# Kernel optimization log

Measured on AMD Instinct MI355X. Metric: run time of the kernel, lower is better.

Reference implementation:

```python
import jax, jax.numpy as jnp
import numpy as np

NODES_PER_GRAPH = 128


def _leaky(x):
    return jnp.where(x >= 0, x, 0.01 * x)


def _graph_conv(x, W, src, dst, w_e, n_nodes):
    # DGL GraphConv, norm='both', bias=False, with edge_weight.
    # Structural (unweighted) degrees, clamped to 1, as in DGL.
    ones = jnp.ones(src.shape[0], dtype=x.dtype)
    deg_out = jnp.clip(jax.ops.segment_sum(ones, src, num_segments=n_nodes), 1.0)
    deg_in = jnp.clip(jax.ops.segment_sum(ones, dst, num_segments=n_nodes), 1.0)
    x = x * (deg_out ** -0.5)[:, None]
    if W.shape[0] > W.shape[1]:  # in_feats > out_feats: project first (DGL order)
        x = x @ W
    msg = x[src] * w_e[:, None]                     # [E, d]
    agg = jax.ops.segment_sum(msg, dst, num_segments=n_nodes)
    agg = agg * (deg_in ** -0.5)[:, None]
    if W.shape[0] <= W.shape[1]:
        agg = agg @ W
    return agg


def setup_inputs() -> dict:
    key = jax.random.key(0)
    ks = jax.random.split(key, 8)
    N, E = 131072, 1048576
    in_feats, hidden, readout = 64, 256, 128
    return {
        "node_feats": jax.random.normal(ks[0], (N, in_feats), dtype=jnp.float32),
        "edge_weight": jax.random.uniform(ks[1], (E,), dtype=jnp.float32),
        "W1": jax.random.normal(ks[2], (in_feats, hidden), dtype=jnp.float32) * 0.1,
        "W2": jax.random.normal(ks[3], (hidden, readout), dtype=jnp.float32) * 0.05,
        "W_lin": jax.random.normal(ks[4], (readout, 64), dtype=jnp.float32) * 0.1,
        "W_cls": jax.random.normal(ks[5], (64, 16), dtype=jnp.float32) * 0.1,
        "edge_src": jax.random.randint(ks[6], (E,), 0, N, dtype=jnp.int32),
        "edge_dst": jax.random.randint(ks[7], (E,), 0, N, dtype=jnp.int32),
    }


def reference(node_feats, edge_weight, W1, W2, W_lin, W_cls, edge_src, edge_dst):
    N = node_feats.shape[0]
    G = N // NODES_PER_GRAPH
    h = _leaky(_graph_conv(node_feats, W1, edge_src, edge_dst, edge_weight, N))
    h = _leaky(_graph_conv(h, W2, edge_src, edge_dst, edge_weight, N))
    # mean_nodes readout over batched graphs of equal size
    gid = jnp.arange(N, dtype=jnp.int32) // NODES_PER_GRAPH
    pooled = jax.ops.segment_sum(h, gid, num_segments=G) / NODES_PER_GRAPH
    # linear -> dropout(eval: identity) -> classifier (no activation in head)
    return (pooled @ W_lin) @ W_cls
```

## Files before the change

kernel.cpp:

```cpp
#include <hip/hip_runtime.h>


constexpr int NPG = 128;
constexpr int F0  = 64;
constexpr int F1  = 256;
constexpr int F2  = 128;
constexpr int BMM = 64;
constexpr int H2  = 136;
constexpr int CAP = 40;
constexpr int NXCD = 8;

using bf16x8 = __attribute__((ext_vector_type(8))) short;
using f32x4  = __attribute__((ext_vector_type(4))) float;
using u16x8  = __attribute__((ext_vector_type(8))) unsigned short;

__device__ __forceinline__ float leaky(float x) {
    return (x >= 0.f) ? x : 0.01f * x;
}

__device__ __forceinline__ unsigned short f2bf(float x) {
    unsigned u = __float_as_uint(x);
    return (unsigned short)((u + 0x7FFFu + ((u >> 16) & 1u)) >> 16);
}
__device__ __forceinline__ float bf2f(unsigned short h) {
    return __uint_as_float(((unsigned)h) << 16);
}
__device__ __forceinline__ void split2(float x, unsigned short& hi, unsigned short& lo) {
    hi = f2bf(x);
    lo = f2bf(x - bf2f(hi));
}

__device__ __forceinline__ f32x4 mfma16(bf16x8 a, bf16x8 b, f32x4 c) {
    return __builtin_amdgcn_mfma_f32_16x16x32_bf16(a, b, c, 0, 0, 0);
}

__device__ __forceinline__ unsigned get_xcc() {
    unsigned xcc;
    asm("s_getreg_b32 %0, hwreg(HW_REG_XCC_ID)" : "=s"(xcc));
    return xcc & (NXCD - 1);
}


__global__ void k_count_fill(const int* __restrict__ src, const int* __restrict__ dst,
                             const float* __restrict__ we,
                             int* __restrict__ cnt_priv,
                             int* __restrict__ cnt_dst,
                             int2* __restrict__ slots, unsigned E, int N) {
    const unsigned xcc = get_xcc();
    unsigned e = blockIdx.x * 256u + threadIdx.x;
    if (e < E) {
        const int s = src[e], d = dst[e];
        const int pos = atomicAdd(&cnt_dst[d], 1);
        if (pos < CAP) slots[(size_t)d * CAP + pos] = make_int2(s, __float_as_int(we[e]));
        __hip_atomic_fetch_add(&cnt_priv[(size_t)xcc * N + s], 1,
                               __ATOMIC_RELAXED, __HIP_MEMORY_SCOPE_WORKGROUP);
    }
}

__global__ void k_finalize_deg(const int* __restrict__ cnt_priv,
                               const int* __restrict__ cnt_dst,
                               float* __restrict__ dinv_out, float* __restrict__ dinv_in,
                               int N) {
    int i = blockIdx.x * blockDim.x + threadIdx.x;
    if (i < N) {
        int c = 0;
#pragma unroll
        for (int x = 0; x < NXCD; ++x) c += cnt_priv[(size_t)x * N + i];
        dinv_out[i] = rsqrtf((float)max(c, 1));
        dinv_in[i]  = rsqrtf((float)max(cnt_dst[i], 1));
    }
}

__global__ void __launch_bounds__(256) k_scale_w(
        int2* __restrict__ slots, const int* __restrict__ cnt_dst,
        const float* __restrict__ dinv_out, int N) {
    int gid = blockIdx.x * 256 + threadIdx.x;
    int n = gid >> 3;
    int j0 = gid & 7;
    if (n >= N) return;
    const int cnt = min(cnt_dst[n], CAP);
    for (int j = j0; j < cnt; j += 8) {
        const size_t idx = (size_t)n * CAP + j;
        int2 p = slots[idx];
        p.y = __float_as_int(__int_as_float(p.y) * dinv_out[p.x]);
        slots[idx] = p;
    }
}

__global__ void k_wsplit1(const float* __restrict__ W1,
                          unsigned short* __restrict__ w1h, unsigned short* __restrict__ w1l) {
    int i = blockIdx.x * 256 + threadIdx.x;
    if (i < F1 * F0) {
        int n = i >> 6, k = i & 63;
        unsigned short h, l;
        split2(W1[k * F1 + n], h, l);
        w1h[i] = h; w1l[i] = l;
    }
}
__global__ void k_wsplit2(const float* __restrict__ W2,
                          unsigned short* __restrict__ w2h, unsigned short* __restrict__ w2l) {
    int i = blockIdx.x * 256 + threadIdx.x;
    if (i < F2 * F1) {
        int n = i >> 8, k = i & 255;
        unsigned short h, l;
        split2(W2[k * F2 + n], h, l);
        w2h[i] = h; w2l[i] = l;
    }
}

__global__ void __launch_bounds__(256) k_gather1(
        const float4* __restrict__ featsv, const int* __restrict__ cnt_dst,
        const int2* __restrict__ slots, const float* __restrict__ dinv_in,
        unsigned short* __restrict__ a1h, unsigned short* __restrict__ a1l, int N) {
    const int gid = blockIdx.x * 256 + threadIdx.x;
    const int n = gid >> 4;
    const int s = gid & 15;
    if (n >= N) return;
    const size_t b = (size_t)n * CAP;
    const int cnt = min(cnt_dst[n], CAP);
    float4 acc = make_float4(0.f, 0.f, 0.f, 0.f);
    int j = 0;
    for (; j + 4 <= cnt; j += 4) {
        const int2 p0 = slots[b + j], p1 = slots[b + j + 1];
        const int2 p2 = slots[b + j + 2], p3 = slots[b + j + 3];
        const float4 v0 = featsv[(size_t)p0.x * 16 + s];
        const float4 v1 = featsv[(size_t)p1.x * 16 + s];
        const float4 v2 = featsv[(size_t)p2.x * 16 + s];
        const float4 v3 = featsv[(size_t)p3.x * 16 + s];
        const float w0 = __int_as_float(p0.y), w1 = __int_as_float(p1.y);
        const float w2 = __int_as_float(p2.y), w3 = __int_as_float(p3.y);
        acc.x = fmaf(v0.x, w0, acc.x); acc.y = fmaf(v0.y, w0, acc.y);
        acc.z = fmaf(v0.z, w0, acc.z); acc.w = fmaf(v0.w, w0, acc.w);
        acc.x = fmaf(v1.x, w1, acc.x); acc.y = fmaf(v1.y, w1, acc.y);
        acc.z = fmaf(v1.z, w1, acc.z); acc.w = fmaf(v1.w, w1, acc.w);
        acc.x = fmaf(v2.x, w2, acc.x); acc.y = fmaf(v2.y, w2, acc.y);
        acc.z = fmaf(v2.z, w2, acc.z); acc.w = fmaf(v2.w, w2, acc.w);
        acc.x = fmaf(v3.x, w3, acc.x); acc.y = fmaf(v3.y, w3, acc.y);
        acc.z = fmaf(v3.z, w3, acc.z); acc.w = fmaf(v3.w, w3, acc.w);
    }
    for (; j < cnt; ++j) {
        const int2 p = slots[b + j];
        const float4 v = featsv[(size_t)p.x * 16 + s];
        const float w = __int_as_float(p.y);
        acc.x = fmaf(v.x, w, acc.x); acc.y = fmaf(v.y, w, acc.y);
        acc.z = fmaf(v.z, w, acc.z); acc.w = fmaf(v.w, w, acc.w);
    }
    const float din = dinv_in[n];
    ushort4 h4, l4;
    split2(acc.x * din, h4.x, l4.x);
    split2(acc.y * din, h4.y, l4.y);
    split2(acc.z * din, h4.z, l4.z);
    split2(acc.w * din, h4.w, l4.w);
    const size_t off = (size_t)n * 64 + s * 4;
    *(ushort4*)(a1h + off) = h4;
    *(ushort4*)(a1l + off) = l4;
}

__global__ void __launch_bounds__(256, 4) k_mfma_fused(
        const unsigned short* __restrict__ a1h, const unsigned short* __restrict__ a1l,
        const unsigned short* __restrict__ w1h, const unsigned short* __restrict__ w1l,
        const unsigned short* __restrict__ w2h, const unsigned short* __restrict__ w2l,
        unsigned short* __restrict__ x2b) {
    __shared__ unsigned short hhi[BMM][H2];
    __shared__ unsigned short hlo[BMM][H2];
    const int tid  = threadIdx.x;
    const int w    = tid >> 6;
    const int lane = tid & 63;
    const int r    = lane & 15;
    const int kg   = lane >> 4;
    const int base = blockIdx.x * BMM;

    f32x4 acc1[4][4] = {};
#pragma unroll
    for (int ks = 0; ks < 2; ++ks) {
        const int kk = ks * 32 + kg * 8;
        bf16x8 wh[4], wl[4];
#pragma unroll
        for (int j = 0; j < 4; ++j) {
            const int col = (j >> 1) * 128 + w * 32 + (j & 1) * 16 + r;
            wh[j] = *(const bf16x8*)(w1h + col * F0 + kk);
            wl[j] = *(const bf16x8*)(w1l + col * F0 + kk);
        }
#pragma unroll
        for (int mt = 0; mt < 4; ++mt) {
            const size_t aoff = (size_t)(base + mt * 16 + r) * F0 + kk;
            const bf16x8 ah = *(const bf16x8*)(a1h + aoff);
            const bf16x8 al = *(const bf16x8*)(a1l + aoff);
#pragma unroll
            for (int j = 0; j < 4; ++j) {
                acc1[mt][j] = mfma16(ah, wh[j], acc1[mt][j]);
                acc1[mt][j] = mfma16(ah, wl[j], acc1[mt][j]);
                acc1[mt][j] = mfma16(al, wh[j], acc1[mt][j]);
            }
        }
    }

    f32x4 acc2[4][2] = {};
    const int c2base = w * 32;
#pragma unroll
    for (int h = 0; h < 2; ++h) {
#pragma unroll
        for (int jn = 0; jn < 2; ++jn) {
            const int j = h * 2 + jn;
            const int lc = w * 32 + jn * 16 + r;
#pragma unroll
            for (int mt = 0; mt < 4; ++mt)
#pragma unroll
                for (int i = 0; i < 4; ++i) {
                    const int rl = mt * 16 + kg * 4 + i;
                    unsigned short hi_, lo_;
                    split2(leaky(acc1[mt][j][i]), hi_, lo_);
                    hhi[rl][lc] = hi_;
                    hlo[rl][lc] = lo_;
                }
        }
        __syncthreads();
#pragma unroll
        for (int ks = 0; ks < 4; ++ks) {
            const int lkk = ks * 32 + kg * 8;
            const int kglob = h * 128 + lkk;
            bf16x8 w2hv[2], w2lv[2];
#pragma unroll
            for (int nt = 0; nt < 2; ++nt) {
                const int col = c2base + nt * 16 + r;
                w2hv[nt] = *(const bf16x8*)(w2h + col * F1 + kglob);
                w2lv[nt] = *(const bf16x8*)(w2l + col * F1 + kglob);
            }
#pragma unroll
            for (int mt = 0; mt < 4; ++mt) {
                const int rl = mt * 16 + r;
                const bf16x8 ah = *(const bf16x8*)&hhi[rl][lkk];
                const bf16x8 al = *(const bf16x8*)&hlo[rl][lkk];
#pragma unroll
                for (int nt = 0; nt < 2; ++nt) {
                    acc2[mt][nt] = mfma16(ah, w2hv[nt], acc2[mt][nt]);
                    acc2[mt][nt] = mfma16(ah, w2lv[nt], acc2[mt][nt]);
                    acc2[mt][nt] = mfma16(al, w2hv[nt], acc2[mt][nt]);
                }
            }
        }
        __syncthreads();
    }

#pragma unroll
    for (int mt = 0; mt < 4; ++mt)
#pragma unroll
        for (int nt = 0; nt < 2; ++nt)
#pragma unroll
            for (int i = 0; i < 4; ++i) {
                const int row = base + mt * 16 + kg * 4 + i;
                const int col = c2base + nt * 16 + r;
                x2b[(size_t)row * F2 + col] = f2bf(acc2[mt][nt][i]);
            }
}

__global__ void __launch_bounds__(256) k_gather2_pool4(
        const ushort* __restrict__ x2b, const int* __restrict__ cnt_dst,
        const int2* __restrict__ slots, const float* __restrict__ dinv_in,
        float* __restrict__ pooled) {
    const int g = blockIdx.x >> 2;
    const int c = blockIdx.x & 3;
    const int t = threadIdx.x;
    const int q = t >> 2;
    const int s = t & 3;
    const int d8 = c * 4 + s;
    const u16x8* x2v = (const u16x8*)x2b;

    float pool[8];
#pragma unroll
    for (int k = 0; k < 8; ++k) pool[k] = 0.f;
    const int nbase = g * NPG;

#pragma unroll
    for (int i = 0; i < NPG; i += 64) {
        const int n = nbase + i + q;
        const size_t b = (size_t)n * CAP;
        const int cnt = min(cnt_dst[n], CAP);
        float a[8];
#pragma unroll
        for (int k = 0; k < 8; ++k) a[k] = 0.f;
        int j = 0;
        for (; j + 4 <= cnt; j += 4) {
            const int2 p0 = slots[b + j], p1 = slots[b + j + 1];
            const int2 p2 = slots[b + j + 2], p3 = slots[b + j + 3];
            const u16x8 u0 = x2v[(size_t)p0.x * 16 + d8];
            const u16x8 u1 = x2v[(size_t)p1.x * 16 + d8];
            const u16x8 u2 = x2v[(size_t)p2.x * 16 + d8];
            const u16x8 u3 = x2v[(size_t)p3.x * 16 + d8];
            const float w0 = __int_as_float(p0.y), w1 = __int_as_float(p1.y);
            const float w2 = __int_as_float(p2.y), w3 = __int_as_float(p3.y);
#pragma unroll
            for (int k = 0; k < 8; ++k) {
                a[k] = fmaf(bf2f(u0[k]), w0, a[k]);
                a[k] = fmaf(bf2f(u1[k]), w1, a[k]);
                a[k] = fmaf(bf2f(u2[k]), w2, a[k]);
                a[k] = fmaf(bf2f(u3[k]), w3, a[k]);
            }
        }
        for (; j < cnt; ++j) {
            const int2 p = slots[b + j];
            const float w = __int_as_float(p.y);
            const u16x8 u = x2v[(size_t)p.x * 16 + d8];
#pragma unroll
            for (int k = 0; k < 8; ++k) a[k] = fmaf(bf2f(u[k]), w, a[k]);
        }
        const float din = dinv_in[n];
#pragma unroll
        for (int k = 0; k < 8; ++k) pool[k] += leaky(a[k] * din);
    }

    __shared__ float pl[64][4][9];
#pragma unroll
    for (int k = 0; k < 8; ++k) pl[q][s][k] = pool[k];
    __syncthreads();
#pragma unroll
    for (int off = 32; off >= 1; off >>= 1) {
        if (q < off) {
#pragma unroll
            for (int k = 0; k < 8; ++k) {
                pool[k] += pl[q + off][s][k];
                pl[q][s][k] = pool[k];
            }
        }
        __syncthreads();
    }
    if (q == 0) {
        const float inv = 1.0f / NPG;
        float* dstp = pooled + (size_t)g * F2 + c * 32 + s * 8;
#pragma unroll
        for (int k = 0; k < 8; ++k) dstp[k] = pool[k] * inv;
    }
}

__global__ void __launch_bounds__(64) k_head(
        const float* __restrict__ pooled,
        const float* __restrict__ Wlin,
        const float* __restrict__ Wcls,
        float* __restrict__ out) {
    const int g = blockIdx.x;
    const int t = threadIdx.x;
    __shared__ float p[F2];
    __shared__ float tj[64];
    p[t]      = pooled[(size_t)g * F2 + t];
    p[t + 64] = pooled[(size_t)g * F2 + 64 + t];
    __syncthreads();
    float s = 0.f;
#pragma unroll
    for (int k = 0; k < F2; ++k) s = fmaf(p[k], Wlin[k * 64 + t], s);
    tj[t] = s;
    __syncthreads();
    if (t < 16) {
        float sum = 0.f;
#pragma unroll
        for (int j = 0; j < 64; ++j) sum = fmaf(tj[j], Wcls[j * 16 + t], sum);
        out[g * 16 + t] = sum;
    }
}

extern "C" void kernel_launch(void* const* d_in, const int* in_sizes, int n_in,
                              void* d_out, int out_size, void* d_ws, size_t ws_size,
                              hipStream_t stream) {
    const float* feats = (const float*)d_in[0];
    const float* we    = (const float*)d_in[1];
    const float* W1    = (const float*)d_in[2];
    const float* W2    = (const float*)d_in[3];
    const float* Wlin  = (const float*)d_in[4];
    const float* Wcls  = (const float*)d_in[5];
    const int*   src   = (const int*)d_in[6];
    const int*   dst   = (const int*)d_in[7];

    const int N = in_sizes[0] / F0;
    const unsigned E = (unsigned)in_sizes[1];
    const int G = N / NPG;

    float* out = (float*)d_out;

    int* ws_i = (int*)d_ws;
    size_t o = 0;
    auto align4 = [&]() { o = (o + 3) & ~(size_t)3; };
    int* cnt_dst = ws_i + o; o += N;
    int* cnt_priv = ws_i + o; o += (size_t)NXCD * N;
    float* dinv_out = (float*)(ws_i + o); o += N;
    float* dinv_in  = (float*)(ws_i + o); o += N;
    align4();
    int2* slots = (int2*)(ws_i + o); o += 2 * (size_t)N * CAP;
    unsigned short* a1h = (unsigned short*)(ws_i + o); o += (size_t)N * 32;
    unsigned short* a1l = (unsigned short*)(ws_i + o); o += (size_t)N * 32;
    unsigned short* x2b = (unsigned short*)(ws_i + o); o += (size_t)N * 64;
    unsigned short* w1h = (unsigned short*)(ws_i + o); o += (F1 * F0) / 2;
    unsigned short* w1l = (unsigned short*)(ws_i + o); o += (F1 * F0) / 2;
    unsigned short* w2h = (unsigned short*)(ws_i + o); o += (F2 * F1) / 2;
    unsigned short* w2l = (unsigned short*)(ws_i + o); o += (F2 * F1) / 2;
    align4();
    float* pooled = (float*)(ws_i + o); o += (size_t)G * F2;

    hipMemsetAsync(cnt_dst, 0, (size_t)(1 + NXCD) * N * sizeof(int), stream);

    k_count_fill<<<(E + 255) / 256, 256, 0, stream>>>(
        src, dst, we, cnt_priv, cnt_dst, slots, E, N);

    k_finalize_deg<<<(N + 255) / 256, 256, 0, stream>>>(
        cnt_priv, cnt_dst, dinv_out, dinv_in, N);

    k_scale_w<<<(N * 8 + 255) / 256, 256, 0, stream>>>(slots, cnt_dst, dinv_out, N);

    k_wsplit1<<<(F1 * F0 + 255) / 256, 256, 0, stream>>>(W1, w1h, w1l);
    k_wsplit2<<<(F2 * F1 + 255) / 256, 256, 0, stream>>>(W2, w2h, w2l);

    k_gather1<<<(N * 16 + 255) / 256, 256, 0, stream>>>(
        (const float4*)feats, cnt_dst, slots, dinv_in, a1h, a1l, N);

    k_mfma_fused<<<N / BMM, 256, 0, stream>>>(a1h, a1l, w1h, w1l, w2h, w2l, x2b);

    k_gather2_pool4<<<G * 4, 256, 0, stream>>>(
        x2b, cnt_dst, slots, dinv_in, pooled);
    k_head<<<G, 64, 0, stream>>>(pooled, Wlin, Wcls, out);
}
```

Before: 317.5 us.

## Gather layer-1 features from a bf16 copy and use nontemporal slot stores

Adds a pre-pass that converts the fp32 node features to bf16, and rewrites the first-layer gather to read 8 bf16 values per lane, which halves the bytes fetched per random neighbour row. The edge-slot fill now packs the source index and weight into one 64-bit value written with a nontemporal store. The change costs an extra conversion pass over the features and gives up precision on the layer-1 inputs, which were previously exact fp32 before the hi/lo split.

```diff
diff --git a/kernel.cpp b/kernel.cpp
--- a/kernel.cpp
+++ b/kernel.cpp
@@ -45,13 +45,17 @@
                              const float* __restrict__ we,
                              int* __restrict__ cnt_priv,
                              int* __restrict__ cnt_dst,
-                             int2* __restrict__ slots, unsigned E, int N) {
+                             long long* __restrict__ slots, unsigned E, int N) {
     const unsigned xcc = get_xcc();
     unsigned e = blockIdx.x * 256u + threadIdx.x;
     if (e < E) {
         const int s = src[e], d = dst[e];
         const int pos = atomicAdd(&cnt_dst[d], 1);
-        if (pos < CAP) slots[(size_t)d * CAP + pos] = make_int2(s, __float_as_int(we[e]));
+        if (pos < CAP) {
+            const long long v = ((long long)(unsigned)__float_as_int(we[e]) << 32)
+                              | (unsigned)s;
+            __builtin_nontemporal_store(v, &slots[(size_t)d * CAP + pos]);
+        }
         __hip_atomic_fetch_add(&cnt_priv[(size_t)xcc * N + s], 1,
                                __ATOMIC_RELAXED, __HIP_MEMORY_SCOPE_WORKGROUP);
     }
@@ -87,6 +91,19 @@
     }
 }
 
+__global__ void __launch_bounds__(256) k_feats_bf(
+        const float4* __restrict__ in, u16x8* __restrict__ out, int total8) {
+    int gid = blockIdx.x * 256 + threadIdx.x;
+    if (gid < total8) {
+        const float4 v0 = in[gid * 2];
+        const float4 v1 = in[gid * 2 + 1];
+        u16x8 r;
+        r[0] = f2bf(v0.x); r[1] = f2bf(v0.y); r[2] = f2bf(v0.z); r[3] = f2bf(v0.w);
+        r[4] = f2bf(v1.x); r[5] = f2bf(v1.y); r[6] = f2bf(v1.z); r[7] = f2bf(v1.w);
+        out[gid] = r;
+    }
+}
+
 __global__ void k_wsplit1(const float* __restrict__ W1,
                           unsigned short* __restrict__ w1h, unsigned short* __restrict__ w1l) {
     int i = blockIdx.x * 256 + threadIdx.x;
@@ -109,51 +126,55 @@
 }
 
 __global__ void __launch_bounds__(256) k_gather1(
-        const float4* __restrict__ featsv, const int* __restrict__ cnt_dst,
+        const u16x8* __restrict__ featsb,
+        const int* __restrict__ cnt_dst,
         const int2* __restrict__ slots, const float* __restrict__ dinv_in,
         unsigned short* __restrict__ a1h, unsigned short* __restrict__ a1l, int N) {
     const int gid = blockIdx.x * 256 + threadIdx.x;
-    const int n = gid >> 4;
-    const int s = gid & 15;
+    const int n = gid >> 3;
+    const int s = gid & 7;
     if (n >= N) return;
     const size_t b = (size_t)n * CAP;
     const int cnt = min(cnt_dst[n], CAP);
-    float4 acc = make_float4(0.f, 0.f, 0.f, 0.f);
+    float a[8];
+#pragma unroll
+    for (int k = 0; k < 8; ++k) a[k] = 0.f;
     int j = 0;
     for (; j + 4 <= cnt; j += 4) {
         const int2 p0 = slots[b + j], p1 = slots[b + j + 1];
         const int2 p2 = slots[b + j + 2], p3 = slots[b + j + 3];
-        const float4 v0 = featsv[(size_t)p0.x * 16 + s];
-        const float4 v1 = featsv[(size_t)p1.x * 16 + s];
-        const float4 v2 = featsv[(size_t)p2.x * 16 + s];
-        const float4 v3 = featsv[(size_t)p3.x * 16 + s];
+        const u16x8 u0 = featsb[(size_t)p0.x * 8 + s];
+        const u16x8 u1 = featsb[(size_t)p1.x * 8 + s];
+        const u16x8 u2 = featsb[(size_t)p2.x * 8 + s];
+        const u16x8 u3 = featsb[(size_t)p3.x * 8 + s];
         const float w0 = __int_as_float(p0.y), w1 = __int_as_float(p1.y);
         const float w2 = __int_as_float(p2.y), w3 = __int_as_float(p3.y);
-        acc.x = fmaf(v0.x, w0, acc.x); acc.y = fmaf(v0.y, w0, acc.y);
-        acc.z = fmaf(v0.z, w0, acc.z); acc.w = fmaf(v0.w, w0, acc.w);
-        acc.x = fmaf(v1.x, w1, acc.x); acc.y = fmaf(v1.y, w1, acc.y);
-        acc.z = fmaf(v1.z, w1, acc.z); acc.w = fmaf(v1.w, w1, acc.w);
-        acc.x = fmaf(v2.x, w2, acc.x); acc.y = fmaf(v2.y, w2, acc.y);
-        acc.z = fmaf(v2.z, w2, acc.z); acc.w = fmaf(v2.w, w2, acc.w);
-        acc.x = fmaf(v3.x, w3, acc.x); acc.y = fmaf(v3.y, w3, acc.y);
-        acc.z = fmaf(v3.z, w3, acc.z); acc.w = fmaf(v3.w, w3, acc.w);
+#pragma unroll
+        for (int k = 0; k < 8; ++k) {
+            a[k] = fmaf(bf2f(u0[k]), w0, a[k]);
+            a[k] = fmaf(bf2f(u1[k]), w1, a[k]);
+            a[k] = fmaf(bf2f(u2[k]), w2, a[k]);
+            a[k] = fmaf(bf2f(u3[k]), w3, a[k]);
+        }
     }
     for (; j < cnt; ++j) {
         const int2 p = slots[b + j];
-        const float4 v = featsv[(size_t)p.x * 16 + s];
+        const u16x8 u = featsb[(size_t)p.x * 8 + s];
         const float w = __int_as_float(p.y);
-        acc.x = fmaf(v.x, w, acc.x); acc.y = fmaf(v.y, w, acc.y);
-        acc.z = fmaf(v.z, w, acc.z); acc.w = fmaf(v.w, w, acc.w);
+#pragma unroll
+        for (int k = 0; k < 8; ++k) a[k] = fmaf(bf2f(u[k]), w, a[k]);
     }
     const float din = dinv_in[n];
-    ushort4 h4, l4;
-    split2(acc.x * din, h4.x, l4.x);
-    split2(acc.y * din, h4.y, l4.y);
-    split2(acc.z * din, h4.z, l4.z);
-    split2(acc.w * din, h4.w, l4.w);
-    const size_t off = (size_t)n * 64 + s * 4;
-    *(ushort4*)(a1h + off) = h4;
-    *(ushort4*)(a1l + off) = l4;
+    u16x8 hv, lv;
+#pragma unroll
+    for (int k = 0; k < 8; ++k) {
+        unsigned short h, l;
+        split2(a[k] * din, h, l);
+        hv[k] = h; lv[k] = l;
+    }
+    const size_t off = (size_t)n * 8 + s;
+    ((u16x8*)a1h)[off] = hv;
+    ((u16x8*)a1l)[off] = lv;
 }
 
 __global__ void __launch_bounds__(256, 4) k_mfma_fused(
@@ -384,6 +405,7 @@
     float* dinv_in  = (float*)(ws_i + o); o += N;
     align4();
     int2* slots = (int2*)(ws_i + o); o += 2 * (size_t)N * CAP;
+    unsigned short* featsb = (unsigned short*)(ws_i + o); o += (size_t)N * 32;
     unsigned short* a1h = (unsigned short*)(ws_i + o); o += (size_t)N * 32;
     unsigned short* a1l = (unsigned short*)(ws_i + o); o += (size_t)N * 32;
     unsigned short* x2b = (unsigned short*)(ws_i + o); o += (size_t)N * 64;
@@ -397,18 +419,21 @@
     hipMemsetAsync(cnt_dst, 0, (size_t)(1 + NXCD) * N * sizeof(int), stream);
 
     k_count_fill<<<(E + 255) / 256, 256, 0, stream>>>(
-        src, dst, we, cnt_priv, cnt_dst, slots, E, N);
+        src, dst, we, cnt_priv, cnt_dst, (long long*)slots, E, N);
 
     k_finalize_deg<<<(N + 255) / 256, 256, 0, stream>>>(
         cnt_priv, cnt_dst, dinv_out, dinv_in, N);
 
     k_scale_w<<<(N * 8 + 255) / 256, 256, 0, stream>>>(slots, cnt_dst, dinv_out, N);
 
+    k_feats_bf<<<(N * 8 + 255) / 256, 256, 0, stream>>>(
+        (const float4*)feats, (u16x8*)featsb, N * 8);
+
     k_wsplit1<<<(F1 * F0 + 255) / 256, 256, 0, stream>>>(W1, w1h, w1l);
     k_wsplit2<<<(F2 * F1 + 255) / 256, 256, 0, stream>>>(W2, w2h, w2l);
 
-    k_gather1<<<(N * 16 + 255) / 256, 256, 0, stream>>>(
-        (const float4*)feats, cnt_dst, slots, dinv_in, a1h, a1l, N);
+    k_gather1<<<(N * 8 + 255) / 256, 256, 0, stream>>>(
+        (const u16x8*)featsb, cnt_dst, slots, dinv_in, a1h, a1l, N);
 
     k_mfma_fused<<<N / BMM, 256, 0, stream>>>(a1h, a1l, w1h, w1l, w2h, w2l, x2b);
 
```

Result: no change. 315.9 us (-0.5%).
